# Performance work log

Hardware: AMD Instinct MI355X
Metric: run time of the kernel (lower is better)

Reference implementation:

```python
import jax, jax.numpy as jnp
import numpy as np

N_NODES = 100000
N_REL = 4
N_EDGES = 500000
D_IN = 128
D_OUT = 128


def setup_inputs() -> dict:
    key = jax.random.key(0)
    k1, k2, k3, k4 = jax.random.split(key, 4)
    x = jax.random.normal(k1, (N_NODES, D_IN), dtype=jnp.float32)
    W = jax.random.normal(k2, (N_REL, D_IN, D_OUT), dtype=jnp.float32) * (1.0 / np.sqrt(D_IN))
    b = jnp.zeros((N_REL, D_OUT), dtype=jnp.float32)
    src_idx = jax.random.randint(k3, (N_REL, N_EDGES), 0, N_NODES)
    dst_idx = jax.random.randint(k4, (N_REL, N_EDGES), 0, N_NODES)
    return {"x": x, "W": W, "b": b, "src_idx": src_idx, "dst_idx": dst_idx}


def reference(x, W, b, src_idx, dst_idx):
    # RGCN layer: per-relation GraphConv(norm='right') -> sum over relations -> ReLU.
    # GraphConv(norm='right'): aggregate src features into dst, divide by dst in-degree,
    # apply weight (in_feats == out_feats so DGL aggregates first, then matmuls), add bias.
    n = x.shape[0]

    def per_relation(src, dst, Wr, br):
        # gather src features [E, D_IN] and scatter-sum into dst rows [N, D_IN]
        agg = jax.ops.segment_sum(x[src], dst, num_segments=n)
        deg = jax.ops.segment_sum(jnp.ones(dst.shape, dtype=x.dtype), dst, num_segments=n)
        agg = agg / jnp.maximum(deg, 1.0)[:, None]  # norm='right'
        return agg @ Wr + br  # [N, D_OUT]

    outs = jax.vmap(per_relation)(src_idx, dst_idx, W, b)  # [R, N, D_OUT]
    h = outs.sum(axis=0)  # HeteroGraphConv aggregate='sum'
    return jax.nn.relu(h)
```

## Files before the change

### kernel.cpp

```cpp
#include <hip/hip_runtime.h>

#define D 128
#define NREL 4
#define BINSHIFT 8
#define NBK 256
#define BCAP 1664
#define CH 4096
#define NBINS_MAX 1600
#define BPT 7

typedef __attribute__((ext_vector_type(8))) short short8;
typedef __attribute__((ext_vector_type(4))) float f32x4;

static __device__ inline unsigned short f2bf(float f) {
    unsigned int u = __float_as_uint(f);
    u += 0x7fffu + ((u >> 16) & 1u);
    return (unsigned short)(u >> 16);
}

__global__ __launch_bounds__(256) void part1prep_kernel(
    const float* __restrict__ x,
    const float* __restrict__ W,
    const float* __restrict__ bias,
    const int* __restrict__ src, const int* __restrict__ dst,
    int* __restrict__ binCnt, unsigned int* __restrict__ part,
    unsigned short* __restrict__ xB,
    unsigned short* __restrict__ Wsw,
    float* __restrict__ bsum,
    int E, int N, int nbins, int total)
{
    __shared__ unsigned int   sh_e[CH];
    __shared__ unsigned short sh_b[CH];
    __shared__ unsigned short sh_inv[CH];
    __shared__ int hist[NBINS_MAX];
    __shared__ int offl[NBINS_MAX];
    __shared__ int basel[NBINS_MAX];
    __shared__ int scanb[256];

    const int t  = threadIdx.x;
    const int E2 = 2 * E, E3 = 3 * E;
    const int nchunks = (total + CH - 1) / CH;

    if (blockIdx.x < nchunks) {
        const int e0 = blockIdx.x * CH;
        const int n  = min(CH, total - e0);

        for (int i = t; i < nbins; i += 256) hist[i] = 0;
        __syncthreads();

        for (int i = t; i < n; i += 256) {
            const int e = e0 + i;
            const int r = (e >= E) + (e >= E2) + (e >= E3);
            const int g = (dst[e] << 2) | r;
            sh_e[i] = (unsigned)src[e] | ((unsigned)(g & (NBK - 1)) << 17);
            const int bin = g >> BINSHIFT;
            sh_b[i] = (unsigned short)bin;
            atomicAdd(&hist[bin], 1);
        }
        __syncthreads();

        int loc[BPT];
        int run = 0;
        #pragma unroll
        for (int k = 0; k < BPT; ++k) {
            const int b = t * BPT + k;
            loc[k] = run;
            run += (b < nbins) ? hist[b] : 0;
        }
        scanb[t] = run;
        __syncthreads();
        for (int off = 1; off < 256; off <<= 1) {
            int v = (t >= off) ? scanb[t - off] : 0;
            __syncthreads();
            scanb[t] += v;
            __syncthreads();
        }
        const int excl = scanb[t] - run;
        #pragma unroll
        for (int k = 0; k < BPT; ++k) {
            const int b = t * BPT + k;
            if (b < nbins) {
                offl[b] = excl + loc[k];
                const int h = hist[b];
                basel[b] = h ? (b * BCAP + atomicAdd(&binCnt[b], h)) : 0;
                hist[b] = 0;
            }
        }
        __syncthreads();

        for (int i = t; i < n; i += 256) {
            const int bin = sh_b[i];
            const int p = offl[bin] + atomicAdd(&hist[bin], 1);
            sh_inv[p] = (unsigned short)i;
        }
        __syncthreads();

        for (int j = t; j < n; j += 256) {
            const int i   = sh_inv[j];
            const int bin = sh_b[i];
            const int dest = basel[bin] + (j - offl[bin]);
            if (dest < (bin + 1) * BCAP)
                part[dest] = sh_e[i];
        }
    }

    const int gtid  = blockIdx.x * 256 + t;
    const int gsize = gridDim.x * 256;

    if (gtid < D)
        bsum[gtid] = bias[gtid] + bias[D + gtid] + bias[2 * D + gtid] + bias[3 * D + gtid];

    for (int gid = gtid; gid < 8192; gid += gsize) {
        const int l   = gid & 63;
        const int ct  = (gid >> 6) & 7;
        const int kb  = gid >> 9;
        const int rel = kb >> 2;
        const int kbase = (kb & 3) * 32 + (l >> 4) * 8;
        const int nn = ct * 16 + (l & 15);
        ushort4 v0, v1;
        const float* wp = W + (size_t)rel * D * D + (size_t)kbase * D + nn;
        v0.x = f2bf(wp[0 * D]); v0.y = f2bf(wp[1 * D]);
        v0.z = f2bf(wp[2 * D]); v0.w = f2bf(wp[3 * D]);
        v1.x = f2bf(wp[4 * D]); v1.y = f2bf(wp[5 * D]);
        v1.z = f2bf(wp[6 * D]); v1.w = f2bf(wp[7 * D]);
        ushort4* op = (ushort4*)(Wsw + (size_t)gid * 8);
        op[0] = v0;
        op[1] = v1;
    }

    const int n4 = N * D / 4;
    for (int i = gtid; i < n4; i += gsize) {
        const float4 v = ((const float4*)x)[i];
        ushort4 o;
        o.x = f2bf(v.x); o.y = f2bf(v.y); o.z = f2bf(v.z); o.w = f2bf(v.w);
        ((ushort4*)xB)[i] = o;
    }
}

__global__ __launch_bounds__(256, 8) void agg_gemm_kernel(
    const unsigned int* __restrict__ part,
    const int* __restrict__ binCnt,
    const unsigned short* __restrict__ xB,
    const unsigned short* __restrict__ Wsw,
    const float* __restrict__ bsum,
    float* __restrict__ out,
    int N)
{
    __shared__ int sh_s[BCAP];
    __shared__ int hist[NBK];
    __shared__ int scanbuf[NBK];
    __shared__ int offl[NBK + 1];
    __shared__ __align__(16) unsigned short agg[32 * 128];
    unsigned int* raw = (unsigned int*)agg;

    const int t    = threadIdx.x;
    const int b    = blockIdx.x;
    const int base = b * BCAP;
    const int cnt  = min(binCnt[b], BCAP);
    const int dst0 = b * 64;

    hist[t] = 0;
    __syncthreads();
    for (int i = t; i < cnt; i += 256) {
        const unsigned v = part[base + i];
        raw[i] = v;
        atomicAdd(&hist[v >> 17], 1);
    }
    __syncthreads();

    const int myc = hist[t];
    scanbuf[t] = myc;
    __syncthreads();
    for (int off = 1; off < 256; off <<= 1) {
        int v = (t >= off) ? scanbuf[t - off] : 0;
        __syncthreads();
        scanbuf[t] += v;
        __syncthreads();
    }
    offl[t] = scanbuf[t] - myc;
    if (t == 255) offl[256] = scanbuf[255];
    hist[t] = scanbuf[t] - myc;
    __syncthreads();

    for (int i = t; i < cnt; i += 256) {
        const unsigned v = raw[i];
        const int pos = atomicAdd(&hist[v >> 17], 1);
        sh_s[pos] = (int)(v & 0x1FFFF);
    }
    __syncthreads();

    const int c    = t & 15;
    const int team = t >> 4;

    const int wv   = t >> 6;
    const int l    = t & 63;
    const int lrow = l & 15;
    const int quad = l >> 4;
    const int ct0  = wv * 2;

    #define ACCUM(v)                                        \
        accL[0] += __uint_as_float((v).x << 16);            \
        accH[0] += __uint_as_float((v).x & 0xffff0000u);    \
        accL[1] += __uint_as_float((v).y << 16);            \
        accH[1] += __uint_as_float((v).y & 0xffff0000u);    \
        accL[2] += __uint_as_float((v).z << 16);            \
        accH[2] += __uint_as_float((v).z & 0xffff0000u);    \
        accL[3] += __uint_as_float((v).w << 16);            \
        accH[3] += __uint_as_float((v).w & 0xffff0000u);

    #pragma unroll 1
    for (int h = 0; h < 2; ++h) {
        f32x4 acc[2][2] = {};

        #pragma unroll 1
        for (int q = 0; q < NREL; ++q) {
            if (h | q) __syncthreads();

            for (int ld = team; ld < 32; ld += 16) {
                const int bkt = (h * 32 + ld) * 4 + q;
                const int beg = offl[bkt];
                const int end = offl[bkt + 1];
                const float inv = 1.0f / fmaxf((float)(end - beg), 1.0f);

                float accL[4] = {0.f, 0.f, 0.f, 0.f};
                float accH[4] = {0.f, 0.f, 0.f, 0.f};

                int j = beg;
                for (; j + 3 < end; j += 4) {
                    const int s0 = sh_s[j];
                    const int s1 = sh_s[j + 1];
                    const int s2 = sh_s[j + 2];
                    const int s3 = sh_s[j + 3];
                    const uint4 v0 = *(const uint4*)(xB + (size_t)s0 * D + c * 8);
                    const uint4 v1 = *(const uint4*)(xB + (size_t)s1 * D + c * 8);
                    const uint4 v2 = *(const uint4*)(xB + (size_t)s2 * D + c * 8);
                    const uint4 v3 = *(const uint4*)(xB + (size_t)s3 * D + c * 8);
                    ACCUM(v0) ACCUM(v1) ACCUM(v2) ACCUM(v3)
                }
                for (; j < end; ++j) {
                    const uint4 v0 = *(const uint4*)(xB + (size_t)sh_s[j] * D + c * 8);
                    ACCUM(v0)
                }

                uint4 o;
                o.x = ((unsigned)f2bf(accH[0] * inv) << 16) | f2bf(accL[0] * inv);
                o.y = ((unsigned)f2bf(accH[1] * inv) << 16) | f2bf(accL[1] * inv);
                o.z = ((unsigned)f2bf(accH[2] * inv) << 16) | f2bf(accL[2] * inv);
                o.w = ((unsigned)f2bf(accH[3] * inv) << 16) | f2bf(accL[3] * inv);
                const int byte = (c * 16) ^ ((ld & 7) << 4);
                *(uint4*)((char*)agg + ld * 256 + byte) = o;
            }
            __syncthreads();

            #pragma unroll
            for (int kbl = 0; kbl < 4; ++kbl) {
                short8 a[2];
                #pragma unroll
                for (int rt = 0; rt < 2; ++rt) {
                    const int row  = rt * 16 + lrow;
                    const int byte = (kbl * 64 + quad * 16) ^ ((row & 7) << 4);
                    a[rt] = *(const short8*)((const char*)agg + row * 256 + byte);
                }
                const int kb = q * 4 + kbl;
                const unsigned short* wp = Wsw + ((size_t)(kb * 8 + ct0) * 64 + l) * 8;
                const short8 b0 = *(const short8*)wp;
                const short8 b1 = *(const short8*)(wp + 64 * 8);
                acc[0][0] = __builtin_amdgcn_mfma_f32_16x16x32_bf16(a[0], b0, acc[0][0], 0, 0, 0);
                acc[1][0] = __builtin_amdgcn_mfma_f32_16x16x32_bf16(a[1], b0, acc[1][0], 0, 0, 0);
                acc[0][1] = __builtin_amdgcn_mfma_f32_16x16x32_bf16(a[0], b1, acc[0][1], 0, 0, 0);
                acc[1][1] = __builtin_amdgcn_mfma_f32_16x16x32_bf16(a[1], b1, acc[1][1], 0, 0, 0);
            }
        }

        #pragma unroll
        for (int ci = 0; ci < 2; ++ci) {
            const int col = (ct0 + ci) * 16 + lrow;
            const float bv = bsum[col];
            #pragma unroll
            for (int rt = 0; rt < 2; ++rt) {
                #pragma unroll
                for (int e = 0; e < 4; ++e) {
                    const int row = dst0 + h * 32 + rt * 16 + quad * 4 + e;
                    if (row < N)
                        out[(size_t)row * D + col] = fmaxf(acc[rt][ci][e] + bv, 0.f);
                }
            }
        }
    }
    #undef ACCUM
}

static inline size_t align_up(size_t v, size_t a) { return (v + a - 1) & ~(a - 1); }

extern "C" void kernel_launch(void* const* d_in, const int* in_sizes, int n_in,
                              void* d_out, int out_size, void* d_ws, size_t ws_size,
                              hipStream_t stream)
{
    const float* x    = (const float*)d_in[0];
    const float* W    = (const float*)d_in[1];
    const float* bias = (const float*)d_in[2];
    const int* src    = (const int*)d_in[3];
    const int* dst    = (const int*)d_in[4];
    float* out        = (float*)d_out;

    const int N = in_sizes[0] / D;
    const int E = in_sizes[3] / NREL;
    const int nG = NREL * N;
    const int totalE = NREL * E;
    const int nbins  = (nG + NBK - 1) >> BINSHIFT;

    char* w = (char*)d_ws;
    int* binCnt = (int*)w;            w += align_up((size_t)nbins * 4, 256);
    unsigned int* part = (unsigned int*)w;     w += align_up((size_t)nbins * BCAP * 4, 256);
    unsigned short* Wsw = (unsigned short*)w;  w += align_up((size_t)512 * D * 2, 256);
    float* bsum = (float*)w;          w += align_up((size_t)D * 4, 256);
    unsigned short* xB = (unsigned short*)w;

    const int nchunks   = (totalE + CH - 1) / CH;
    const int p1_blocks = nchunks > 1024 ? nchunks : 1024;

    hipMemsetAsync(binCnt, 0, (size_t)nbins * sizeof(int), stream);
    part1prep_kernel<<<p1_blocks, 256, 0, stream>>>(
        x, W, bias, src, dst, binCnt, part, xB, Wsw, bsum, E, N, nbins, totalE);
    agg_gemm_kernel<<<nbins, 256, 0, stream>>>(part, binCnt, xB, Wsw, bsum, out, N);
}
```

Baseline: 280.2 us.

## Replace LDS-staged chunk binning with direct per-edge global atomic binning

The partition kernel stops staging 4096-edge chunks in shared memory with a local histogram, scan and reorder before writing to bins. Each thread now reads src/dst as int4, does one global atomicAdd per edge on the bin counter, and writes the entry straight into the bin slot. This removes the many block barriers and the large LDS footprint that limited occupancy. In exchange it issues 2M global atomics contended across about 1563 counters and makes scattered, uncoalesced writes to part.

```diff
diff --git a/kernel.cpp b/kernel.cpp
--- a/kernel.cpp
+++ b/kernel.cpp
@@ -5,9 +5,6 @@
 #define BINSHIFT 8
 #define NBK 256
 #define BCAP 1664
-#define CH 4096
-#define NBINS_MAX 1600
-#define BPT 7
 
 typedef __attribute__((ext_vector_type(8))) short short8;
 typedef __attribute__((ext_vector_type(4))) float f32x4;
@@ -29,83 +26,39 @@
     float* __restrict__ bsum,
     int E, int N, int nbins, int total)
 {
-    __shared__ unsigned int   sh_e[CH];
-    __shared__ unsigned short sh_b[CH];
-    __shared__ unsigned short sh_inv[CH];
-    __shared__ int hist[NBINS_MAX];
-    __shared__ int offl[NBINS_MAX];
-    __shared__ int basel[NBINS_MAX];
-    __shared__ int scanb[256];
-
-    const int t  = threadIdx.x;
-    const int E2 = 2 * E, E3 = 3 * E;
-    const int nchunks = (total + CH - 1) / CH;
-
-    if (blockIdx.x < nchunks) {
-        const int e0 = blockIdx.x * CH;
-        const int n  = min(CH, total - e0);
-
-        for (int i = t; i < nbins; i += 256) hist[i] = 0;
-        __syncthreads();
-
-        for (int i = t; i < n; i += 256) {
-            const int e = e0 + i;
-            const int r = (e >= E) + (e >= E2) + (e >= E3);
-            const int g = (dst[e] << 2) | r;
-            sh_e[i] = (unsigned)src[e] | ((unsigned)(g & (NBK - 1)) << 17);
-            const int bin = g >> BINSHIFT;
-            sh_b[i] = (unsigned short)bin;
-            atomicAdd(&hist[bin], 1);
-        }
-        __syncthreads();
-
-        int loc[BPT];
-        int run = 0;
-        #pragma unroll
-        for (int k = 0; k < BPT; ++k) {
-            const int b = t * BPT + k;
-            loc[k] = run;
-            run += (b < nbins) ? hist[b] : 0;
-        }
-        scanb[t] = run;
-        __syncthreads();
-        for (int off = 1; off < 256; off <<= 1) {
-            int v = (t >= off) ? scanb[t - off] : 0;
-            __syncthreads();
-            scanb[t] += v;
-            __syncthreads();
-        }
-        const int excl = scanb[t] - run;
-        #pragma unroll
-        for (int k = 0; k < BPT; ++k) {
-            const int b = t * BPT + k;
-            if (b < nbins) {
-                offl[b] = excl + loc[k];
-                const int h = hist[b];
-                basel[b] = h ? (b * BCAP + atomicAdd(&binCnt[b], h)) : 0;
-                hist[b] = 0;
-            }
-        }
-        __syncthreads();
-
-        for (int i = t; i < n; i += 256) {
-            const int bin = sh_b[i];
-            const int p = offl[bin] + atomicAdd(&hist[bin], 1);
-            sh_inv[p] = (unsigned short)i;
-        }
-        __syncthreads();
-
-        for (int j = t; j < n; j += 256) {
-            const int i   = sh_inv[j];
-            const int bin = sh_b[i];
-            const int dest = basel[bin] + (j - offl[bin]);
-            if (dest < (bin + 1) * BCAP)
-                part[dest] = sh_e[i];
-        }
-    }
-
+    const int t     = threadIdx.x;
     const int gtid  = blockIdx.x * 256 + t;
     const int gsize = gridDim.x * 256;
+    const int E2 = 2 * E, E3 = 3 * E;
+
+    const int nq = total >> 2;
+    for (int i = gtid; i < nq; i += gsize) {
+        const int e = i * 4;
+        const int4 s4 = ((const int4*)src)[i];
+        const int4 d4 = ((const int4*)dst)[i];
+        #pragma unroll
+        for (int k = 0; k < 4; ++k) {
+            const int ek = e + k;
+            const int sk = (k == 0) ? s4.x : (k == 1) ? s4.y : (k == 2) ? s4.z : s4.w;
+            const int dk = (k == 0) ? d4.x : (k == 1) ? d4.y : (k == 2) ? d4.z : d4.w;
+            const int r  = (ek >= E) + (ek >= E2) + (ek >= E3);
+            const int g  = (dk << 2) | r;
+            const unsigned entry = (unsigned)sk | ((unsigned)(g & (NBK - 1)) << 17);
+            const int bin = g >> BINSHIFT;
+            const int pos = atomicAdd(&binCnt[bin], 1);
+            if (pos < BCAP)
+                part[(size_t)bin * BCAP + pos] = entry;
+        }
+    }
+    for (int e = (nq << 2) + gtid; e < total; e += gsize) {
+        const int r  = (e >= E) + (e >= E2) + (e >= E3);
+        const int g  = (dst[e] << 2) | r;
+        const unsigned entry = (unsigned)src[e] | ((unsigned)(g & (NBK - 1)) << 17);
+        const int bin = g >> BINSHIFT;
+        const int pos = atomicAdd(&binCnt[bin], 1);
+        if (pos < BCAP)
+            part[(size_t)bin * BCAP + pos] = entry;
+    }
 
     if (gtid < D)
         bsum[gtid] = bias[gtid] + bias[D + gtid] + bias[2 * D + gtid] + bias[3 * D + gtid];
@@ -155,7 +108,7 @@
 
     const int t    = threadIdx.x;
     const int b    = blockIdx.x;
-    const int base = b * BCAP;
+    const size_t base = (size_t)b * BCAP;
     const int cnt  = min(binCnt[b], BCAP);
     const int dst0 = b * 64;
 
@@ -316,8 +269,7 @@
     float* bsum = (float*)w;          w += align_up((size_t)D * 4, 256);
     unsigned short* xB = (unsigned short*)w;
 
-    const int nchunks   = (totalE + CH - 1) / CH;
-    const int p1_blocks = nchunks > 1024 ? nchunks : 1024;
+    const int p1_blocks = 2048;
 
     hipMemsetAsync(binCnt, 0, (size_t)nbins * sizeof(int), stream);
     part1prep_kernel<<<p1_blocks, 256, 0, stream>>>(
```

Result: slower. 487.6 us (+74.0%).
